# Kernel tuning notes

Hardware: AMD Instinct MI355X
Metric: run time of the kernel (lower is better)

## Reference

```python
import jax, jax.numpy as jnp
import numpy as np

B, S, H, NH = 2, 2048, 1024, 16


def setup_inputs() -> dict:
    key = jax.random.key(0)
    ks = jax.random.split(key, 5)
    x = jax.random.normal(ks[0], (B, S, H), dtype=jnp.float32)
    # causal mask: True = attend
    mask = jnp.tril(jnp.ones((S, S), dtype=bool))[None, None, :, :]
    scale = 1.0 / np.sqrt(H)
    Wq = jax.random.normal(ks[1], (H, H), dtype=jnp.float32) * scale
    Wk = jax.random.normal(ks[2], (H, H), dtype=jnp.float32) * scale
    Wv = jax.random.normal(ks[3], (H, H), dtype=jnp.float32) * scale
    Wo = jax.random.normal(ks[4], (H, H), dtype=jnp.float32) * scale
    return {"x": x, "mask": mask, "Wq": Wq, "Wk": Wk, "Wv": Wv, "Wo": Wo}


def _split_heads(t, n_heads):
    b, s, h = t.shape
    return t.reshape(b, s, n_heads, h // n_heads).transpose(0, 2, 1, 3)  # (b,h,s,d)


def reference(x, mask, Wq, Wk, Wv, Wo):
    q = _split_heads(x @ Wq, NH)
    k = _split_heads(x @ Wk, NH)
    v = _split_heads(x @ Wv, NH)
    d_head = q.shape[-1]
    scores = jnp.einsum('bhqd,bhkd->bhqk', q, k) / jnp.sqrt(jnp.asarray(d_head, q.dtype))
    neg = jnp.asarray(jnp.finfo(scores.dtype).min, scores.dtype)
    scores = jnp.where(mask, scores, neg)  # mask_to_bias: True->0 bias, False->-inf
    attn = jax.nn.softmax(scores, axis=-1)
    out = jnp.einsum('bhqk,bhkd->bhqd', attn, v)
    out = out.transpose(0, 2, 1, 3).reshape(x.shape[0], x.shape[1], -1)  # merge heads
    return out @ Wo
```

## Files before the change

### kernel.cpp

```cpp
#include <hip/hip_runtime.h>

using u16 = unsigned short;
typedef __attribute__((ext_vector_type(8))) __bf16 bf16x8;
typedef __attribute__((ext_vector_type(4))) float f32x4;
typedef __attribute__((ext_vector_type(8))) u16 u16x8;
typedef __attribute__((ext_vector_type(4))) u16 u16x4;
typedef __attribute__((ext_vector_type(4))) float floatx4;

__device__ __forceinline__ u16 f2b(float f) {
    __bf16 h = (__bf16)f;
    return __builtin_bit_cast(u16, h);
}

__device__ __forceinline__ void gload16(const void* g, void* l) {
    __builtin_amdgcn_global_load_lds((const __attribute__((address_space(1))) void*)g,
                                     (__attribute__((address_space(3))) void*)l, 16, 0, 0);
}

constexpr int Hdim = 1024, Bdim = 2, Sdim = 2048, Dh = 64;
constexpr int NTOK = Bdim * Sdim;

__global__ void cast_x_kernel(const float* __restrict__ x, u16* __restrict__ xb, int n4) {
    int i = blockIdx.x * blockDim.x + threadIdx.x;
    int stride = gridDim.x * blockDim.x;
    for (; i < n4; i += stride) {
        floatx4 v = reinterpret_cast<const floatx4*>(x)[i];
        u16x4 o;
        #pragma unroll
        for (int j = 0; j < 4; ++j) o[j] = f2b(v[j]);
        reinterpret_cast<u16x4*>(xb)[i] = o;
    }
}

__global__ void transpose_cast_w(const float* __restrict__ W0, const float* __restrict__ W1,
                                 const float* __restrict__ W2, const float* __restrict__ W3,
                                 u16* __restrict__ T0, u16* __restrict__ T1,
                                 u16* __restrict__ T2, u16* __restrict__ T3) {
    __shared__ float tile[32][33];
    const float* W; u16* T;
    switch (blockIdx.z) {
        case 0: W = W0; T = T0; break;
        case 1: W = W1; T = T1; break;
        case 2: W = W2; T = T2; break;
        default: W = W3; T = T3; break;
    }
    int bx = blockIdx.x * 32, by = blockIdx.y * 32;
    int tx = threadIdx.x, ty = threadIdx.y;
    #pragma unroll
    for (int i = 0; i < 4; ++i)
        tile[ty + i * 8][tx] = W[(size_t)(by + ty + i * 8) * Hdim + bx + tx];
    __syncthreads();
    #pragma unroll
    for (int i = 0; i < 4; ++i)
        T[(size_t)(bx + ty + i * 8) * Hdim + by + tx] = f2b(tile[tx][ty + i * 8]);
}

template <int MODE, int BN>
__global__ __launch_bounds__(256) void gemm_bt(const u16* __restrict__ A, const u16* __restrict__ Bt,
                                               void* __restrict__ C0, void* __restrict__ C1,
                                               void* __restrict__ C2, int N, int K) {
    constexpr int NB = BN / 32;
    __shared__ __align__(16) u16 As[128 * 32];
    __shared__ __align__(16) u16 Bs[BN * 32];
    const int tid = threadIdx.x;
    const int lane = tid & 63, wid = tid >> 6;
    const int wr = wid >> 1, wc = wid & 1;
    const int fr = lane & 15, g = lane >> 4, k8 = g * 8;
    const int rowBase = blockIdx.y * 128, colBase = blockIdx.x * BN;
    const int sr = lane >> 2, sc = (lane & 3) * 8;
    f32x4 acc[4][NB] = {};
    for (int k0 = 0; k0 < K; k0 += 32) {
        __syncthreads();
        #pragma unroll
        for (int i = 0; i < 2; ++i) {
            const int rb = wid * 32 + i * 16;
            gload16(&A[(size_t)(rowBase + rb + sr) * K + k0 + sc], &As[rb * 32]);
        }
        if constexpr (BN == 128) {
            #pragma unroll
            for (int i = 0; i < 2; ++i) {
                const int rb = wid * 32 + i * 16;
                gload16(&Bt[(size_t)(colBase + rb + sr) * K + k0 + sc], &Bs[rb * 32]);
            }
        } else {
            const int rb = wid * 16;
            gload16(&Bt[(size_t)(colBase + rb + sr) * K + k0 + sc], &Bs[rb * 32]);
        }
        __syncthreads();
        bf16x8 af[4], bfr[NB];
        #pragma unroll
        for (int m = 0; m < 4; ++m)
            af[m] = *reinterpret_cast<const bf16x8*>(&As[(wr * 64 + m * 16 + fr) * 32 + k8]);
        #pragma unroll
        for (int n = 0; n < NB; ++n)
            bfr[n] = *reinterpret_cast<const bf16x8*>(&Bs[(wc * (BN / 2) + n * 16 + fr) * 32 + k8]);
        #pragma unroll
        for (int m = 0; m < 4; ++m)
            #pragma unroll
            for (int n = 0; n < NB; ++n)
                acc[m][n] = __builtin_amdgcn_mfma_f32_16x16x32_bf16(af[m], bfr[n], acc[m][n], 0, 0, 0);
    }
    #pragma unroll
    for (int m = 0; m < 4; ++m) {
        #pragma unroll
        for (int n = 0; n < NB; ++n) {
            const int row = rowBase + wr * 64 + m * 16 + g * 4;
            const int col = colBase + wc * (BN / 2) + n * 16 + fr;
            if constexpr (MODE == 0) {
                u16* C = (u16*)C0;
                #pragma unroll
                for (int j = 0; j < 4; ++j) C[(size_t)(row + j) * N + col] = f2b(acc[m][n][j]);
            } else if constexpr (MODE == 1) {
                float* C = (float*)C0;
                #pragma unroll
                for (int j = 0; j < 4; ++j) C[(size_t)(row + j) * N + col] = acc[m][n][j];
            } else {
                if (col < 1024) {
                    u16* Qm = (u16*)C0;
                    #pragma unroll
                    for (int j = 0; j < 4; ++j) Qm[(size_t)(row + j) * 1024 + col] = f2b(acc[m][n][j]);
                } else if (col < 2048) {
                    u16* Km = (u16*)C1;
                    #pragma unroll
                    for (int j = 0; j < 4; ++j) Km[(size_t)(row + j) * 1024 + (col - 1024)] = f2b(acc[m][n][j]);
                } else {
                    u16* Vt = (u16*)C2;
                    u16x4 pk;
                    #pragma unroll
                    for (int j = 0; j < 4; ++j) pk[j] = f2b(acc[m][n][j]);
                    *reinterpret_cast<u16x4*>(&Vt[(size_t)(col - 2048) * NTOK + row]) = pk;
                }
            }
        }
    }
}

__global__ __launch_bounds__(256, 2) void attn_kernel(const u16* __restrict__ Q, const u16* __restrict__ Km,
                                                      const u16* __restrict__ VtG, u16* __restrict__ AO) {
    __shared__ __align__(16) u16 Kt[2][64 * 64];
    __shared__ __align__(16) u16 Vt[2][64 * 64];
    __shared__ __align__(16) u16 Pw[4][16][72];
    const int tid = threadIdx.x, lane = tid & 63, w = tid >> 6;
    const int bid = blockIdx.x;
    const int xg = bid & 7, rem = bid >> 3;
    const int p = rem & 15, yg = rem >> 4;
    const int grp = xg + 8 * yg;
    const int h = grp & 15, b = grp >> 4;
    const int qsel[2] = { p, 31 - p };
    const int h0 = h * Dh;
    const size_t boff = (size_t)b * Sdim * Hdim;
    const u16* Qb = Q + boff;
    u16* AOb = AO + boff;
    const int fr = lane & 15, g = lane >> 4;

    const int lr = lane >> 3;
    const int lc8 = ((lane & 7) ^ lr) * 8;
    const u16* Kg = Km + boff + (size_t)(w * 8 + lr) * Hdim + h0 + lc8;
    const u16* Vg = VtG + (size_t)(h0 + w * 8 + lr) * NTOK + (size_t)b * Sdim + lc8;

    auto stage = [&](int t, int bufi) {
        const int kv0 = t * 64;
        #pragma unroll
        for (int i = 0; i < 2; ++i) {
            gload16(Kg + (size_t)(kv0 + i * 32) * Hdim, &Kt[bufi][w * 512 + i * 2048]);
            gload16(Vg + (size_t)(i * 32) * NTOK + kv0, &Vt[bufi][w * 512 + i * 2048]);
        }
    };

    constexpr float QSCALE = 0.125f * 1.44269504089f;
    bf16x8 qf[2][2];
    int qrow0[2];
    #pragma unroll
    for (int m = 0; m < 2; ++m) {
        qrow0[m] = qsel[m] * 64 + w * 16;
        #pragma unroll
        for (int c = 0; c < 2; ++c) {
            bf16x8 t = *reinterpret_cast<const bf16x8*>(
                &Qb[(size_t)(qrow0[m] + fr) * Hdim + h0 + c * 32 + g * 8]);
            bf16x8 r;
            #pragma unroll
            for (int j = 0; j < 8; ++j) r[j] = (__bf16)((float)t[j] * QSCALE);
            qf[m][c] = r;
        }
    }

    f32x4 o[2][4] = {};
    float mrow[2] = { -INFINITY, -INFINITY };
    float lrow[2] = { 0.f, 0.f };

    const int ntiles = qsel[1] + 1;
    stage(0, 0);
    __syncthreads();
    int buf = 0;
    for (int t = 0; t < ntiles; ++t) {
        if (t + 1 < ntiles) stage(t + 1, buf ^ 1);
        const int kv0 = t * 64;
        #pragma unroll
        for (int m = 0; m < 2; ++m) {
            if (t > qsel[m]) continue;
            const bool masked = (t == qsel[m]);
            f32x4 s[4];
            __builtin_amdgcn_s_setprio(1);
            #pragma unroll
            for (int n = 0; n < 4; ++n) {
                const int row = n * 16 + fr;
                const int sw = (row & 7) << 3;
                const u16* kp = &Kt[buf][row * 64];
                bf16x8 kf0 = *reinterpret_cast<const bf16x8*>(&kp[(g * 8) ^ sw]);
                bf16x8 kf1 = *reinterpret_cast<const bf16x8*>(&kp[(32 + g * 8) ^ sw]);
                f32x4 z = {};
                z = __builtin_amdgcn_mfma_f32_16x16x32_bf16(kf0, qf[m][0], z, 0, 0, 0);
                s[n] = __builtin_amdgcn_mfma_f32_16x16x32_bf16(kf1, qf[m][1], z, 0, 0, 0);
            }
            __builtin_amdgcn_s_setprio(0);
            if (masked) {
                const int qr = qrow0[m] + fr;
                #pragma unroll
                for (int n = 0; n < 4; ++n)
                    #pragma unroll
                    for (int j = 0; j < 4; ++j) {
                        const int kv = kv0 + n * 16 + g * 4 + j;
                        if (kv > qr) s[n][j] = -3.0e38f;
                    }
            }
            float mx = -3.0e38f;
            #pragma unroll
            for (int n = 0; n < 4; ++n)
                mx = fmaxf(mx, fmaxf(fmaxf(s[n][0], s[n][1]), fmaxf(s[n][2], s[n][3])));
            mx = fmaxf(mx, __shfl_xor(mx, 16));
            mx = fmaxf(mx, __shfl_xor(mx, 32));
            const bool skip = (__all(mx <= mrow[m] + 8.0f) != 0);
            const float mnew = skip ? mrow[m] : fmaxf(mrow[m], mx);
            float rs = 0.f;
            #pragma unroll
            for (int n = 0; n < 4; ++n) {
                u16x4 pk;
                #pragma unroll
                for (int j = 0; j < 4; ++j) {
                    const float pv = exp2f(s[n][j] - mnew);
                    rs += pv;
                    pk[j] = f2b(pv);
                }
                *reinterpret_cast<u16x4*>(&Pw[w][fr][n * 16 + g * 4]) = pk;
            }
            rs += __shfl_xor(rs, 16);
            rs += __shfl_xor(rs, 32);
            if (skip) {
                lrow[m] += rs;
            } else {
                const float alpha = exp2f(mrow[m] - mnew);
                lrow[m] = lrow[m] * alpha + rs;
                mrow[m] = mnew;
                #pragma unroll
                for (int j = 0; j < 4; ++j) {
                    const float aj = __shfl(alpha, g * 4 + j);
                    #pragma unroll
                    for (int n = 0; n < 4; ++n) o[m][n][j] *= aj;
                }
            }
            bf16x8 pa0 = *reinterpret_cast<const bf16x8*>(&Pw[w][fr][g * 8]);
            bf16x8 pa1 = *reinterpret_cast<const bf16x8*>(&Pw[w][fr][32 + g * 8]);
            __builtin_amdgcn_s_setprio(1);
            #pragma unroll
            for (int n = 0; n < 4; ++n) {
                const int row = n * 16 + fr;
                const int sw = (row & 7) << 3;
                const u16* vp = &Vt[buf][row * 64];
                bf16x8 vf0 = *reinterpret_cast<const bf16x8*>(&vp[(g * 8) ^ sw]);
                bf16x8 vf1 = *reinterpret_cast<const bf16x8*>(&vp[(32 + g * 8) ^ sw]);
                o[m][n] = __builtin_amdgcn_mfma_f32_16x16x32_bf16(pa0, vf0, o[m][n], 0, 0, 0);
                o[m][n] = __builtin_amdgcn_mfma_f32_16x16x32_bf16(pa1, vf1, o[m][n], 0, 0, 0);
            }
            __builtin_amdgcn_s_setprio(0);
        }
        __syncthreads();
        buf ^= 1;
    }

    #pragma unroll
    for (int m = 0; m < 2; ++m) {
        const float invl = 1.0f / lrow[m];
        #pragma unroll
        for (int j = 0; j < 4; ++j) {
            const float ij = __shfl(invl, g * 4 + j);
            const int qrow = qrow0[m] + g * 4 + j;
            #pragma unroll
            for (int n = 0; n < 4; ++n)
                AOb[(size_t)qrow * Hdim + h0 + n * 16 + fr] = f2b(o[m][n][j] * ij);
        }
    }
}

extern "C" void kernel_launch(void* const* d_in, const int* in_sizes, int n_in,
                              void* d_out, int out_size, void* d_ws, size_t ws_size,
                              hipStream_t stream) {
    const float* x  = (const float*)d_in[0];
    const float* Wq = (const float*)d_in[2];
    const float* Wk = (const float*)d_in[3];
    const float* Wv = (const float*)d_in[4];
    const float* Wo = (const float*)d_in[5];
    float* out = (float*)d_out;

    u16* ws  = (u16*)d_ws;
    u16* Xb  = ws;
    u16* WqT = ws  + 4194304;
    u16* WkT = WqT + 1048576;
    u16* WvT = WkT + 1048576;
    u16* WoT = WvT + 1048576;
    u16* Qm  = WoT + 1048576;
    u16* Km  = Qm  + 4194304;
    u16* Vt  = Km  + 4194304;
    u16* AO  = Vt  + 4194304;

    cast_x_kernel<<<2048, 256, 0, stream>>>(x, Xb, NTOK * Hdim / 4);
    transpose_cast_w<<<dim3(32, 32, 4), dim3(32, 8), 0, stream>>>(Wq, Wk, Wv, Wo, WqT, WkT, WvT, WoT);
    gemm_bt<2, 128><<<dim3(24, 32), 256, 0, stream>>>(Xb, WqT, Qm, Km, Vt, 3072, Hdim);
    attn_kernel<<<dim3(512), 256, 0, stream>>>(Qm, Km, Vt, AO);
    gemm_bt<1, 64><<<dim3(16, 32), 256, 0, stream>>>(AO, WoT, out, nullptr, nullptr, Hdim, Hdim);
}
```

Before: 208.0 us.

## Add dedicated double-buffered QKV GEMM with swizzled LDS and K=64 stages

Replaces the generic gemm_bt QKV projection with a dedicated kernel that double-buffers LDS tiles, using direct global-to-LDS loads for the next K step while computing the current one. It widens each K step to 64 and applies an XOR swizzle on LDS columns to reduce bank conflicts on fragment reads. The aim is to hide global load latency and halve the number of barriers in the largest GEMM. In exchange it uses 64KB of LDS per block, which may lower occupancy.

```diff
diff --git a/kernel.cpp b/kernel.cpp
--- a/kernel.cpp
+++ b/kernel.cpp
@@ -53,6 +53,81 @@
     #pragma unroll
     for (int i = 0; i < 4; ++i)
         T[(size_t)(bx + ty + i * 8) * Hdim + by + tx] = f2b(tile[tx][ty + i * 8]);
+}
+
+__global__ __launch_bounds__(256) void gemm_qkv(const u16* __restrict__ A, const u16* __restrict__ Bt,
+                                                u16* __restrict__ Qm, u16* __restrict__ Km,
+                                                u16* __restrict__ Vt, int K) {
+    __shared__ __align__(16) u16 As[2][128 * 64];
+    __shared__ __align__(16) u16 Bs[2][128 * 64];
+    const int tid = threadIdx.x, lane = tid & 63, wid = tid >> 6;
+    const int wr = wid >> 1, wc = wid & 1;
+    const int fr = lane & 15, g = lane >> 4;
+    const int rowBase = blockIdx.y * 128, colBase = blockIdx.x * 128;
+    const int srow = lane >> 3;
+    const int scol = ((lane & 7) ^ srow) * 8;
+    const u16* Ag = A + (size_t)(rowBase + srow) * K + scol;
+    const u16* Bg = Bt + (size_t)(colBase + srow) * K + scol;
+
+    auto stage = [&](int s, int bufi) {
+        const int k0 = s * 64;
+        #pragma unroll
+        for (int i = 0; i < 4; ++i) {
+            const int r = i * 32 + wid * 8;
+            gload16(Ag + (size_t)r * K + k0, &As[bufi][r * 64]);
+            gload16(Bg + (size_t)r * K + k0, &Bs[bufi][r * 64]);
+        }
+    };
+
+    f32x4 acc[4][4] = {};
+    stage(0, 0);
+    __syncthreads();
+    int buf = 0;
+    const int nsteps = K / 64;
+    for (int s = 0; s < nsteps; ++s) {
+        if (s + 1 < nsteps) stage(s + 1, buf ^ 1);
+        #pragma unroll
+        for (int kk = 0; kk < 2; ++kk) {
+            bf16x8 bfr[4];
+            #pragma unroll
+            for (int n = 0; n < 4; ++n) {
+                const int row = wc * 64 + n * 16 + fr;
+                bfr[n] = *reinterpret_cast<const bf16x8*>(
+                    &Bs[buf][row * 64 + ((kk * 32 + g * 8) ^ ((row & 7) << 3))]);
+            }
+            #pragma unroll
+            for (int m = 0; m < 4; ++m) {
+                const int row = wr * 64 + m * 16 + fr;
+                bf16x8 af = *reinterpret_cast<const bf16x8*>(
+                    &As[buf][row * 64 + ((kk * 32 + g * 8) ^ ((row & 7) << 3))]);
+                #pragma unroll
+                for (int n = 0; n < 4; ++n)
+                    acc[m][n] = __builtin_amdgcn_mfma_f32_16x16x32_bf16(af, bfr[n], acc[m][n], 0, 0, 0);
+            }
+        }
+        __syncthreads();
+        buf ^= 1;
+    }
+    #pragma unroll
+    for (int m = 0; m < 4; ++m) {
+        #pragma unroll
+        for (int n = 0; n < 4; ++n) {
+            const int row = rowBase + wr * 64 + m * 16 + g * 4;
+            const int col = colBase + wc * 64 + n * 16 + fr;
+            if (col < 1024) {
+                #pragma unroll
+                for (int j = 0; j < 4; ++j) Qm[(size_t)(row + j) * 1024 + col] = f2b(acc[m][n][j]);
+            } else if (col < 2048) {
+                #pragma unroll
+                for (int j = 0; j < 4; ++j) Km[(size_t)(row + j) * 1024 + (col - 1024)] = f2b(acc[m][n][j]);
+            } else {
+                u16x4 pk;
+                #pragma unroll
+                for (int j = 0; j < 4; ++j) pk[j] = f2b(acc[m][n][j]);
+                *reinterpret_cast<u16x4*>(&Vt[(size_t)(col - 2048) * NTOK + row]) = pk;
+            }
+        }
+    }
 }
 
 template <int MODE, int BN>
@@ -110,26 +185,10 @@
                 u16* C = (u16*)C0;
                 #pragma unroll
                 for (int j = 0; j < 4; ++j) C[(size_t)(row + j) * N + col] = f2b(acc[m][n][j]);
-            } else if constexpr (MODE == 1) {
+            } else {
                 float* C = (float*)C0;
                 #pragma unroll
                 for (int j = 0; j < 4; ++j) C[(size_t)(row + j) * N + col] = acc[m][n][j];
-            } else {
-                if (col < 1024) {
-                    u16* Qm = (u16*)C0;
-                    #pragma unroll
-                    for (int j = 0; j < 4; ++j) Qm[(size_t)(row + j) * 1024 + col] = f2b(acc[m][n][j]);
-                } else if (col < 2048) {
-                    u16* Km = (u16*)C1;
-                    #pragma unroll
-                    for (int j = 0; j < 4; ++j) Km[(size_t)(row + j) * 1024 + (col - 1024)] = f2b(acc[m][n][j]);
-                } else {
-                    u16* Vt = (u16*)C2;
-                    u16x4 pk;
-                    #pragma unroll
-                    for (int j = 0; j < 4; ++j) pk[j] = f2b(acc[m][n][j]);
-                    *reinterpret_cast<u16x4*>(&Vt[(size_t)(col - 2048) * NTOK + row]) = pk;
-                }
             }
         }
     }
@@ -314,7 +373,7 @@
 
     cast_x_kernel<<<2048, 256, 0, stream>>>(x, Xb, NTOK * Hdim / 4);
     transpose_cast_w<<<dim3(32, 32, 4), dim3(32, 8), 0, stream>>>(Wq, Wk, Wv, Wo, WqT, WkT, WvT, WoT);
-    gemm_bt<2, 128><<<dim3(24, 32), 256, 0, stream>>>(Xb, WqT, Qm, Km, Vt, 3072, Hdim);
+    gemm_qkv<<<dim3(24, 32), 256, 0, stream>>>(Xb, WqT, Qm, Km, Vt, Hdim);
     attn_kernel<<<dim3(512), 256, 0, stream>>>(Qm, Km, Vt, AO);
     gemm_bt<1, 64><<<dim3(16, 32), 256, 0, stream>>>(AO, WoT, out, nullptr, nullptr, Hdim, Hdim);
 }
```

Result: no change. 208.7 us (+0.3%).
